# Optimization experiments

Hardware: AMD Instinct MI355X
Metric: run time of the kernel (lower is better)

The kernel has to match this reference:

```python
import jax, jax.numpy as jnp
import numpy as np

B, N, C = 8, 2048, 64  # batch, num nodes, channels
DENSITY = 0.01


def setup_inputs() -> dict:
    key = jax.random.key(0)
    k = jax.random.split(key, 8)
    x = jax.random.normal(k[0], (B, N, C), dtype=jnp.float32)

    # --- replicate sym_norm_Adj(Adj_matrix) + row softmax from __init__ ---
    W = (jax.random.uniform(k[1], (N, N)) < DENSITY).astype(jnp.float32)
    W = W + 0.5 * jnp.eye(N, dtype=jnp.float32)          # W + 0.5*I
    deg = jnp.sum((W != 0.0).astype(jnp.float32), axis=1)  # row nonzero counts
    A = jnp.sqrt(deg)[:, None] * W * jnp.sqrt(deg)[None, :]  # sqrt(D) W sqrt(D)
    A = jax.nn.softmax(A, axis=1)

    s = 1.0 / np.sqrt(C)
    Wq = jax.random.normal(k[2], (C, C), dtype=jnp.float32) * s   # stored as (in,out)
    Wk = jax.random.normal(k[3], (C, C), dtype=jnp.float32) * s
    Wv = jax.random.normal(k[4], (C, N), dtype=jnp.float32) * s   # c_in -> num_node
    theta_w = jax.random.normal(k[5], (C, C), dtype=jnp.float32) * s
    theta_b = jnp.zeros((C,), dtype=jnp.float32)
    alpha = jnp.array([0.95], dtype=jnp.float32)
    beta = jnp.array([0.95], dtype=jnp.float32)
    return {"x": x, "A": A, "Wq": Wq, "Wk": Wk, "Wv": Wv,
            "theta_w": theta_w, "theta_b": theta_b, "alpha": alpha, "beta": beta}


def reference(x, A, Wq, Wk, Wv, theta_w, theta_b, alpha, beta):
    # Spatial_Attention_layer
    Q = x @ Wq                                   # (B,N,C)
    K = x @ Wk                                   # (B,N,C)
    V = x @ Wv                                   # (B,N,N)
    score = jnp.einsum('bnc,bmc->bnm', Q, K)     # (B,N,N)
    score = jax.nn.softmax(score, axis=1)        # softmax over dim=1 (as in torch code)
    spat = jnp.einsum('bnm,bmk->bnk', score, V)  # (B,N,N) spatial attention

    # einsum('nn,bnc->bnc', A, x) == diag(A) broadcast-multiply
    static_out = jnp.diagonal(A)[None, :, None] * x  # (B,N,C)

    # dy_adj = A @ spat; einsum('bnn,bnc->bnc', dy_adj, x) uses only diag(dy_adj)
    dy_diag = jnp.einsum('nj,bjn->bn', A, spat)      # (B,N), avoids (B,N,N) intermediate
    dy_out = (dy_diag[:, :, None] * x) @ theta_w + theta_b  # Theta1 linear

    out = jax.nn.relu(alpha[0] * static_out + beta[0] * dy_out)
    return out
```

## Files before the change

### kernel.cpp

```cpp
#include <hip/hip_runtime.h>

constexpr int Bb = 8;
constexpr int Nn = 2048;
constexpr int Cc = 64;
constexpr int CAPS = 192;

typedef __attribute__((ext_vector_type(4))) float f32x4;
typedef __attribute__((ext_vector_type(16))) float f32x16;
typedef __attribute__((ext_vector_type(8))) short bf16x8;
typedef __attribute__((ext_vector_type(4))) unsigned u32x4;

__device__ inline unsigned short f2bf(float f){
  unsigned u = __builtin_bit_cast(unsigned, f);
  unsigned r = (u + 0x7FFFu + ((u>>16)&1u)) >> 16;
  return (unsigned short)r;
}
__device__ inline float bf2f(unsigned short h){
  unsigned u = ((unsigned)h)<<16; return __builtin_bit_cast(float,u);
}
__device__ inline unsigned pk2(float a, float b){
  return (unsigned)f2bf(a) | ((unsigned)f2bf(b)<<16);
}

typedef __attribute__((address_space(1))) unsigned GU32;
typedef __attribute__((address_space(3))) unsigned LU32;
__device__ inline void load_lds16(const void* g, void* l){
  __builtin_amdgcn_global_load_lds((const GU32*)g, (LU32*)l, 16, 0, 0);
}

__device__ inline size_t qk_chunk(int b, int s, int q, int l){
  return ((((size_t)b*64 + s)*4 + q)*64 + l)*8;
}
__device__ inline size_t xz_chunk(int b, int mq, int cb, int l){
  return ((((size_t)b*128 + mq)*2 + cb)*64 + l)*8;
}

#define MFMA32(a,b,c) __builtin_amdgcn_mfma_f32_32x32x16_bf16(a,b,c,0,0,0)

__global__ __launch_bounds__(256) void mega_k(
    const float* __restrict__ x, const float* __restrict__ A,
    const float* __restrict__ Wq, const float* __restrict__ Wk,
    const float* __restrict__ Tw, const float* __restrict__ Wv,
    unsigned short* __restrict__ Qhi, unsigned short* __restrict__ Qlo,
    unsigned short* __restrict__ Khi, unsigned short* __restrict__ Klo,
    float* __restrict__ xt, float* __restrict__ Xp,
    float* __restrict__ r_, float* __restrict__ diagA, int* __restrict__ cnt,
    int* __restrict__ idx, float* __restrict__ val,
    float* __restrict__ WvT, unsigned short* __restrict__ xf){
  __shared__ __attribute__((aligned(16))) char smem[65792];
  int blk = blockIdx.x; int t = threadIdx.x;

  if(blk < 256){
    float* wql = (float*)smem;
    float* wkl = wql + 4096;
    float* twl = wkl + 4096;
    float (*xr)[64] = (float(*)[64])(twl + 4096);
    float* xsl = (float*)(xr + 64);
    #pragma unroll
    for(int i=0;i<4;i++){
      *(f32x4*)&wql[i*1024+t*4] = *(const f32x4*)&Wq[i*1024+t*4];
      *(f32x4*)&wkl[i*1024+t*4] = *(const f32x4*)&Wk[i*1024+t*4];
      *(f32x4*)&twl[i*1024+t*4] = *(const f32x4*)&Tw[i*1024+t*4];
    }
    if(t<64) xsl[t]=0.f;
    long long row0 = (long long)blk*64;
    int r = t>>4, q = t&15, c0 = q*4;
    #pragma unroll
    for(int i=0;i<4;i++){
      int row = i*16 + r;
      *(f32x4*)&xr[row][c0] = *(const f32x4*)&x[(row0+row)*Cc + c0];
    }
    __syncthreads();
    f32x4 aq[4], ak[4], at4[4];
    #pragma unroll
    for(int g=0;g<4;g++){ aq[g]=(f32x4){0,0,0,0}; ak[g]=(f32x4){0,0,0,0}; at4[g]=(f32x4){0,0,0,0}; }
    for(int kk=0;kk<64;kk++){
      f32x4 wq4 = *(const f32x4*)&wql[kk*64+c0];
      f32x4 wk4 = *(const f32x4*)&wkl[kk*64+c0];
      f32x4 wt4 = *(const f32x4*)&twl[kk*64+c0];
      #pragma unroll
      for(int g=0;g<4;g++){
        float xv = xr[g*16+r][kk];
        aq[g] += xv*wq4; ak[g] += xv*wk4; at4[g] += xv*wt4;
      }
    }
    float xsp[4] = {0.f,0.f,0.f,0.f};
    int q2 = c0>>4, hb = (c0>>3)&1, cs = c0&7;
    #pragma unroll
    for(int g=0;g<4;g++){
      #pragma unroll
      for(int d=0;d<4;d++) xsp[d] += xr[g*16+r][c0+d];
      long long rg = row0 + g*16 + r;
      unsigned long long hq=0,lq=0,hk=0,lk=0;
      #pragma unroll
      for(int d=0;d<4;d++){
        float v = aq[g][d];
        unsigned short h = f2bf(v); unsigned short lo2 = f2bf(v - bf2f(h));
        hq |= (unsigned long long)h << (16*d); lq |= (unsigned long long)lo2 << (16*d);
        v = ak[g][d];
        h = f2bf(v); lo2 = f2bf(v - bf2f(h));
        hk |= (unsigned long long)h << (16*d); lk |= (unsigned long long)lo2 << (16*d);
      }
      int b2 = (int)(rg>>11); int s2 = ((int)rg>>5)&63;
      int l2 = ((int)rg&31) + 32*hb;
      size_t off = qk_chunk(b2, s2, q2, l2) + cs;
      *(unsigned long long*)&Qhi[off] = hq;
      *(unsigned long long*)&Qlo[off] = lq;
      *(unsigned long long*)&Khi[off] = hk;
      *(unsigned long long*)&Klo[off] = lk;
      *(f32x4*)&xt[rg*Cc + c0] = at4[g];
    }
    __syncthreads();
    #pragma unroll
    for(int d=0;d<4;d++) atomicAdd(&xsl[c0+d], xsp[d]);
    __syncthreads();
    if(t<64) Xp[blk*64+t] = xsl[t];
    {
      int b2 = blk>>5; int m0 = (blk&31)*64;
      #pragma unroll
      for(int i=0;i<2;i++){
        int k2 = i*256 + t; int mg2 = k2>>6; int c = k2&63;
        int mloc = mg2*8;
        unsigned u0 = pk2(xr[mloc+0][c], xr[mloc+1][c]);
        unsigned u1 = pk2(xr[mloc+2][c], xr[mloc+3][c]);
        unsigned u2 = pk2(xr[mloc+4][c], xr[mloc+5][c]);
        unsigned u3 = pk2(xr[mloc+6][c], xr[mloc+7][c]);
        u32x4 uu = {u0,u1,u2,u3};
        int mq = (m0 + mloc)>>4; int cb = c>>5; int l2 = (c&31) + 32*(mg2&1);
        *(u32x4*)(xf + xz_chunk(b2, mq, cb, l2)) = uu;
      }
    }
  } else if(blk < 768){
    int n = (blk-256)*4 + (t>>6); int l = t&63;
    const float* row = A + (size_t)n*Nn;
    float mn = 1e30f;
    for(int j=l;j<Nn;j+=64) mn = fminf(mn, row[j]);
    #pragma unroll
    for(int off=32;off>=1;off>>=1) mn = fminf(mn, __shfl_xor(mn,off));
    float thr = mn*1.3f;
    int bse=0;
    for(int j0=0;j0<Nn;j0+=64){
      float v = row[j0+l];
      bool f = v>thr;
      unsigned long long m = __ballot(f);
      int pos = __popcll(m & ((1ull<<l)-1ull));
      if(f && bse+pos<CAPS){ idx[n*CAPS+bse+pos]=j0+l; val[n*CAPS+bse+pos]=v-mn; }
      bse += __popcll(m);
    }
    if(l==0){ r_[n]=mn; diagA[n]=row[n]; cnt[n] = bse<CAPS? bse : CAPS; }
  } else {
    float (*tile)[65] = (float(*)[65])smem;
    int n0 = (blk-768)*64;
    for(int i=0;i<16;i++){
      int cc = i*4 + (t>>6); int nn2 = t&63;
      tile[cc][nn2] = Wv[(size_t)cc*Nn + n0 + nn2];
    }
    __syncthreads();
    for(int i=0;i<16;i++){
      int nn2 = i*4 + (t>>6); int cc = t&63;
      WvT[(size_t)(n0+nn2)*Cc + cc] = tile[cc][nn2];
    }
  }
}

__global__ __launch_bounds__(256,2) void zpass_k(
    const unsigned short* __restrict__ Qhi, const unsigned short* __restrict__ Qlo,
    const unsigned short* __restrict__ Khi, const unsigned short* __restrict__ Klo,
    float* __restrict__ Zp){
  __shared__ uint4 stg[2][512];
  int id = blockIdx.x;
  int b = id&7; int mg = (id>>3)&15; int jq = id>>7;
  int t = threadIdx.x, w = t>>6, l = t&63;
  int mt = mg*4 + w;
  bf16x8 Kh[4], Kl4[4];
  #pragma unroll
  for(int q=0;q<4;q++){
    Kh[q]  = *(const bf16x8*)(Khi + qk_chunk(b, mt, q, l));
    Kl4[q] = *(const bf16x8*)(Klo + qk_chunk(b, mt, q, l));
  }
  char* wbase0 = (char*)&stg[0][0] + (t>>6)*1024;
  char* wbase1 = (char*)&stg[1][0] + (t>>6)*1024;
  {
    int s = jq*8;
    load_lds16(Qhi + qk_chunk(b,s,0,0) + t*8, wbase0);
    load_lds16(Qlo + qk_chunk(b,s,0,0) + t*8, wbase0 + 4096);
  }
  __syncthreads();
  float zacc = 0.f;
  for(int it=0; it<8; it++){
    int buf = it&1;
    if(it+1<8){
      int s = jq*8 + it + 1;
      char* wb = buf? wbase0 : wbase1;
      load_lds16(Qhi + qk_chunk(b,s,0,0) + t*8, wb);
      load_lds16(Qlo + qk_chunk(b,s,0,0) + t*8, wb + 4096);
    }
    f32x16 sa, sb;
    #pragma unroll
    for(int r=0;r<16;r++){ sa[r]=0.f; sb[r]=0.f; }
    #pragma unroll
    for(int q=0;q<4;q++){
      bf16x8 Qh4 = *(const bf16x8*)&stg[buf][q*64 + l];
      bf16x8 Ql4 = *(const bf16x8*)&stg[buf][256 + q*64 + l];
      sa = MFMA32(Qh4, Kh[q],  sa);
      sb = MFMA32(Ql4, Kh[q],  sb);
      sb = MFMA32(Qh4, Kl4[q], sb);
    }
    float p = 0.f;
    #pragma unroll
    for(int r=0;r<16;r++) p += __expf(sa[r]+sb[r]);
    zacc += p;
    __syncthreads();
  }
  zacc += __shfl_down(zacc, 32);
  if(l<32) Zp[((size_t)(jq*8 + b))*Nn + mt*32 + l] = zacc;
}

__global__ __launch_bounds__(256,2) void fused_k(
    const unsigned short* __restrict__ Qhi, const unsigned short* __restrict__ Qlo,
    const unsigned short* __restrict__ Khi, const unsigned short* __restrict__ Klo,
    const unsigned short* __restrict__ xf, const float* __restrict__ Zp,
    float* __restrict__ Pp){
  __shared__ uint4 stg[2][768];
  __shared__ float lniz[256];
  int id = blockIdx.x;
  int b = id&7; int jb = (id>>3)&15; int mo = id>>7;
  int t = threadIdx.x, w = t>>6, l = t&63, lr = l&31, hh = l>>5;
  int js = jb*4 + w;
  {
    int m = mo*256 + t;
    float z = 0.f;
    #pragma unroll
    for(int p=0;p<8;p++) z += Zp[((size_t)(p*8 + b))*Nn + m];
    lniz[t] = -__logf(z);
  }
  bf16x8 Qh4[4], Ql4[4];
  #pragma unroll
  for(int q=0;q<4;q++){
    Qh4[q] = *(const bf16x8*)(Qhi + qk_chunk(b, js, q, l));
    Ql4[q] = *(const bf16x8*)(Qlo + qk_chunk(b, js, q, l));
  }
  char* wbase0 = (char*)&stg[0][0] + (t>>6)*1024;
  char* wbase1 = (char*)&stg[1][0] + (t>>6)*1024;
  {
    int s = mo*8;
    load_lds16(Khi + qk_chunk(b,s,0,0) + t*8, wbase0);
    load_lds16(Klo + qk_chunk(b,s,0,0) + t*8, wbase0 + 4096);
    load_lds16(xf + xz_chunk(b,2*s,0,0) + t*8, wbase0 + 8192);
  }
  __syncthreads();
  f32x16 pa0, pa1;
  #pragma unroll
  for(int r=0;r<16;r++){ pa0[r]=0.f; pa1[r]=0.f; }
  for(int it=0; it<8; it++){
    int buf = it&1;
    if(it+1<8){
      int s = mo*8 + it + 1;
      char* wb = buf? wbase0 : wbase1;
      load_lds16(Khi + qk_chunk(b,s,0,0) + t*8, wb);
      load_lds16(Klo + qk_chunk(b,s,0,0) + t*8, wb + 4096);
      load_lds16(xf + xz_chunk(b,2*s,0,0) + t*8, wb + 8192);
    }
    f32x16 sa, sb;
    #pragma unroll
    for(int r=0;r<16;r++){ sa[r]=0.f; sb[r]=0.f; }
    #pragma unroll
    for(int q=0;q<4;q++){
      bf16x8 Kh4 = *(const bf16x8*)&stg[buf][q*64 + l];
      bf16x8 Kl4 = *(const bf16x8*)&stg[buf][256 + q*64 + l];
      sa = MFMA32(Kh4, Qh4[q], sa);
      sb = MFMA32(Kl4, Qh4[q], sb);
      sb = MFMA32(Kh4, Ql4[q], sb);
    }
    bf16x8 b00 = *(const bf16x8*)&stg[buf][512 + l];
    bf16x8 b10 = *(const bf16x8*)&stg[buf][512 + 64 + l];
    bf16x8 b01 = *(const bf16x8*)&stg[buf][512 + 128 + l];
    bf16x8 b11 = *(const bf16x8*)&stg[buf][512 + 192 + l];
    float e[16];
    #pragma unroll
    for(int r=0;r<16;r++){
      int mrow = (r&3) + 8*(r>>2) + 4*hh;
      e[r] = __expf(sa[r] + sb[r] + lniz[it*32 + mrow]);
    }
    unsigned wd0,wd1,wd2,wd3,wd4,wd5,wd6,wd7;
    {
      unsigned x0 = pk2(e[0],  e[1]);
      unsigned x1 = pk2(e[2],  e[3]);
      unsigned y0 = pk2(e[4],  e[5]);
      unsigned y1 = pk2(e[6],  e[7]);
      asm("v_permlane32_swap_b32 %0, %1" : "+v"(x0), "+v"(y0));
      asm("v_permlane32_swap_b32 %0, %1" : "+v"(x1), "+v"(y1));
      wd0=x0; wd1=x1; wd2=y0; wd3=y1;
      unsigned x2 = pk2(e[8],  e[9]);
      unsigned x3 = pk2(e[10], e[11]);
      unsigned y2 = pk2(e[12], e[13]);
      unsigned y3 = pk2(e[14], e[15]);
      asm("v_permlane32_swap_b32 %0, %1" : "+v"(x2), "+v"(y2));
      asm("v_permlane32_swap_b32 %0, %1" : "+v"(x3), "+v"(y3));
      wd4=x2; wd5=x3; wd6=y2; wd7=y3;
    }
    u32x4 u1 = {wd0,wd1,wd2,wd3};
    u32x4 u2 = {wd4,wd5,wd6,wd7};
    bf16x8 f1 = __builtin_bit_cast(bf16x8, u1);
    bf16x8 f2 = __builtin_bit_cast(bf16x8, u2);
    pa0 = MFMA32(f1, b00, pa0);
    pa0 = MFMA32(f2, b01, pa0);
    pa1 = MFMA32(f1, b10, pa1);
    pa1 = MFMA32(f2, b11, pa1);
    __syncthreads();
  }
  float* Pb = Pp + ((size_t)(mo*8 + b)*Nn + js*32)*Cc;
  #pragma unroll
  for(int r=0;r<16;r++){
    int jr = (r&3) + 8*(r>>2) + 4*hh;
    Pb[(size_t)jr*Cc + lr]      = pa0[r];
    Pb[(size_t)jr*Cc + 32 + lr] = pa1[r];
  }
}

__global__ __launch_bounds__(256) void psum_k(const float* __restrict__ Pp,
                                              float* __restrict__ P){
  size_t i = ((size_t)blockIdx.x*256 + threadIdx.x)*4;
  const size_t st = (size_t)Bb*Nn*Cc;
  f32x4 s0 = *(const f32x4*)(Pp + i)        + *(const f32x4*)(Pp + st + i);
  f32x4 s1 = *(const f32x4*)(Pp + 2*st + i) + *(const f32x4*)(Pp + 3*st + i);
  f32x4 s2 = *(const f32x4*)(Pp + 4*st + i) + *(const f32x4*)(Pp + 5*st + i);
  f32x4 s3 = *(const f32x4*)(Pp + 6*st + i) + *(const f32x4*)(Pp + 7*st + i);
  *(f32x4*)(P + i) = (s0+s1)+(s2+s3);
}

__global__ __launch_bounds__(256) void final_k(const float* __restrict__ x,
    const float* __restrict__ xt, const float* __restrict__ P,
    const float* __restrict__ WvT, const float* __restrict__ Xp,
    const float* __restrict__ r_, const float* __restrict__ diagA,
    const int* __restrict__ cnt, const int* __restrict__ idx,
    const float* __restrict__ val, const float* __restrict__ tb,
    const float* __restrict__ alp, const float* __restrict__ bet,
    float* __restrict__ out){
  int t=threadIdx.x; int l=t&63;
  int bn = blockIdx.x*4 + (t>>6);
  int b = bn>>11, n = bn&2047;
  float wv = WvT[n*Cc+l];
  float xs = 0.f;
  const float* xpb = Xp + (size_t)b*32*Cc;
  #pragma unroll 8
  for(int p=0;p<32;p++) xs += xpb[p*Cc + l];
  float tacc = r_[n]*xs;
  int cn = cnt[n];
  const float* Pb = P + (size_t)b*Nn*Cc;
  const int* ix = idx + n*CAPS;
  const float* vl = val + n*CAPS;
  for(int k=0;k<cn;k++)
    tacc += vl[k] * Pb[(size_t)ix[k]*Cc + l];
  float d = wv*tacc;
  #pragma unroll
  for(int off=32;off>=1;off>>=1) d += __shfl_xor(d,off);
  size_t g = (size_t)bn*Cc + l;
  float o = alp[0]*diagA[n]*x[g] + bet[0]*(d*xt[g] + tb[l]);
  out[g] = fmaxf(o,0.f);
}

extern "C" void kernel_launch(void* const* d_in, const int* in_sizes, int n_in,
                              void* d_out, int out_size, void* d_ws, size_t ws_size,
                              hipStream_t stream){
  const float* x  = (const float*)d_in[0];
  const float* A  = (const float*)d_in[1];
  const float* Wq = (const float*)d_in[2];
  const float* Wk = (const float*)d_in[3];
  const float* Wv = (const float*)d_in[4];
  const float* Tw = (const float*)d_in[5];
  const float* tb = (const float*)d_in[6];
  const float* alp= (const float*)d_in[7];
  const float* bet= (const float*)d_in[8];
  float* out = (float*)d_out;

  char* base = (char*)d_ws; size_t off=0;
  auto al=[&](size_t sz)->void*{ void* q = base+off; off=(off+sz+255)&~(size_t)255; return q; };
  unsigned short* Qhi=(unsigned short*)al((size_t)Bb*Nn*Cc*2);
  unsigned short* Qlo=(unsigned short*)al((size_t)Bb*Nn*Cc*2);
  unsigned short* Khi=(unsigned short*)al((size_t)Bb*Nn*Cc*2);
  unsigned short* Klo=(unsigned short*)al((size_t)Bb*Nn*Cc*2);
  float* xt  =(float*)al((size_t)Bb*Nn*Cc*4);
  float* Pp  =(float*)al((size_t)8*Bb*Nn*Cc*4);
  float* P   =(float*)al((size_t)Bb*Nn*Cc*4);
  float* Zp  =(float*)al((size_t)8*Bb*Nn*4);
  float* Xp  =(float*)al((size_t)256*Cc*4);
  float* WvT =(float*)al((size_t)Nn*Cc*4);
  float* r_  =(float*)al((size_t)Nn*4);
  float* dgA =(float*)al((size_t)Nn*4);
  int*   cnt =(int*)al((size_t)Nn*4);
  int*   idx =(int*)al((size_t)Nn*CAPS*4);
  float* val =(float*)al((size_t)Nn*CAPS*4);
  unsigned short* xf=(unsigned short*)al((size_t)Bb*Cc*Nn*2);
  (void)ws_size;

  mega_k<<<800, 256, 0, stream>>>(x, A, Wq, Wk, Tw, Wv,
      Qhi, Qlo, Khi, Klo, xt, Xp, r_, dgA, cnt, idx, val, WvT, xf);
  zpass_k<<<1024, 256, 0, stream>>>(Qhi,Qlo,Khi,Klo,Zp);
  fused_k<<<1024, 256, 0, stream>>>(Qhi,Qlo,Khi,Klo,xf,Zp,Pp);
  psum_k<<<(int)((size_t)Bb*Nn*Cc/4/256), 256, 0, stream>>>(Pp,P);
  final_k<<<Bb*Nn/4, 256, 0, stream>>>(x,xt,P,WvT,Xp,r_,dgA,cnt,idx,val,tb,alp,bet,out);
}
```

Measured before the change: 109.8 us.

## Triple-buffer LDS prefetch in zpass/fused and halve fused_k m-splits

Both attention passes move from double-buffered LDS staging with a full syncthreads per iteration to a three-stage ring, using explicit vmcnt waits plus a raw s_barrier so two tiles stay in flight. fused_k now processes 16 m-tiles per block instead of 8 and launches half as many blocks. That halves the partial-P buffer and the work left for psum_k, which now sums four slices. The cost is more LDS per block, fewer blocks to fill the GPU, and hand-written waitcnt fences that rely on the exact ordering of async loads.

```diff
diff --git a/kernel.cpp b/kernel.cpp
--- a/kernel.cpp
+++ b/kernel.cpp
@@ -27,6 +27,12 @@
 __device__ inline void load_lds16(const void* g, void* l){
   __builtin_amdgcn_global_load_lds((const GU32*)g, (LU32*)l, 16, 0, 0);
 }
+
+#define PIPE_FENCE_N(N) do{ \
+    asm volatile("s_waitcnt vmcnt(" #N ")" ::: "memory"); \
+    __builtin_amdgcn_sched_barrier(0); \
+    __builtin_amdgcn_s_barrier(); \
+    __builtin_amdgcn_sched_barrier(0); }while(0)
 
 __device__ inline size_t qk_chunk(int b, int s, int q, int l){
   return ((((size_t)b*64 + s)*4 + q)*64 + l)*8;
@@ -167,7 +173,7 @@
     const unsigned short* __restrict__ Qhi, const unsigned short* __restrict__ Qlo,
     const unsigned short* __restrict__ Khi, const unsigned short* __restrict__ Klo,
     float* __restrict__ Zp){
-  __shared__ uint4 stg[2][512];
+  __shared__ uint4 stg[3][512];
   int id = blockIdx.x;
   int b = id&7; int mg = (id>>3)&15; int jq = id>>7;
   int t = threadIdx.x, w = t>>6, l = t&63;
@@ -178,30 +184,24 @@
     Kh[q]  = *(const bf16x8*)(Khi + qk_chunk(b, mt, q, l));
     Kl4[q] = *(const bf16x8*)(Klo + qk_chunk(b, mt, q, l));
   }
-  char* wbase0 = (char*)&stg[0][0] + (t>>6)*1024;
-  char* wbase1 = (char*)&stg[1][0] + (t>>6)*1024;
-  {
-    int s = jq*8;
-    load_lds16(Qhi + qk_chunk(b,s,0,0) + t*8, wbase0);
-    load_lds16(Qlo + qk_chunk(b,s,0,0) + t*8, wbase0 + 4096);
-  }
-  __syncthreads();
+#define ZISSUE(S, BI) { \
+    char* wb = (char*)&stg[BI][0] + ((t>>6)<<10); \
+    load_lds16(Qhi + qk_chunk(b,(S),0,0) + t*8, wb); \
+    load_lds16(Qlo + qk_chunk(b,(S),0,0) + t*8, wb + 4096); }
+  ZISSUE(jq*8,   0);
+  ZISSUE(jq*8+1, 1);
   float zacc = 0.f;
+  #pragma unroll
   for(int it=0; it<8; it++){
-    int buf = it&1;
-    if(it+1<8){
-      int s = jq*8 + it + 1;
-      char* wb = buf? wbase0 : wbase1;
-      load_lds16(Qhi + qk_chunk(b,s,0,0) + t*8, wb);
-      load_lds16(Qlo + qk_chunk(b,s,0,0) + t*8, wb + 4096);
-    }
+    const int bi = it%3;
+    if(it==7) PIPE_FENCE_N(0); else PIPE_FENCE_N(2);
     f32x16 sa, sb;
     #pragma unroll
     for(int r=0;r<16;r++){ sa[r]=0.f; sb[r]=0.f; }
     #pragma unroll
     for(int q=0;q<4;q++){
-      bf16x8 Qh4 = *(const bf16x8*)&stg[buf][q*64 + l];
-      bf16x8 Ql4 = *(const bf16x8*)&stg[buf][256 + q*64 + l];
+      bf16x8 Qh4 = *(const bf16x8*)&stg[bi][q*64 + l];
+      bf16x8 Ql4 = *(const bf16x8*)&stg[bi][256 + q*64 + l];
       sa = MFMA32(Qh4, Kh[q],  sa);
       sb = MFMA32(Ql4, Kh[q],  sb);
       sb = MFMA32(Qh4, Kl4[q], sb);
@@ -210,8 +210,9 @@
     #pragma unroll
     for(int r=0;r<16;r++) p += __expf(sa[r]+sb[r]);
     zacc += p;
-    __syncthreads();
-  }
+    if(it+2<8) ZISSUE(jq*8+it+2, (it+2)%3);
+  }
+#undef ZISSUE
   zacc += __shfl_down(zacc, 32);
   if(l<32) Zp[((size_t)(jq*8 + b))*Nn + mt*32 + l] = zacc;
 }
@@ -221,18 +222,19 @@
     const unsigned short* __restrict__ Khi, const unsigned short* __restrict__ Klo,
     const unsigned short* __restrict__ xf, const float* __restrict__ Zp,
     float* __restrict__ Pp){
-  __shared__ uint4 stg[2][768];
-  __shared__ float lniz[256];
+  __shared__ uint4 stg[3][768];
+  __shared__ float lniz[512];
   int id = blockIdx.x;
   int b = id&7; int jb = (id>>3)&15; int mo = id>>7;
   int t = threadIdx.x, w = t>>6, l = t&63, lr = l&31, hh = l>>5;
   int js = jb*4 + w;
-  {
-    int m = mo*256 + t;
+  #pragma unroll
+  for(int i=0;i<2;i++){
+    int m = mo*512 + i*256 + t;
     float z = 0.f;
     #pragma unroll
     for(int p=0;p<8;p++) z += Zp[((size_t)(p*8 + b))*Nn + m];
-    lniz[t] = -__logf(z);
+    lniz[i*256+t] = -__logf(z);
   }
   bf16x8 Qh4[4], Ql4[4];
   #pragma unroll
@@ -240,42 +242,36 @@
     Qh4[q] = *(const bf16x8*)(Qhi + qk_chunk(b, js, q, l));
     Ql4[q] = *(const bf16x8*)(Qlo + qk_chunk(b, js, q, l));
   }
-  char* wbase0 = (char*)&stg[0][0] + (t>>6)*1024;
-  char* wbase1 = (char*)&stg[1][0] + (t>>6)*1024;
-  {
-    int s = mo*8;
-    load_lds16(Khi + qk_chunk(b,s,0,0) + t*8, wbase0);
-    load_lds16(Klo + qk_chunk(b,s,0,0) + t*8, wbase0 + 4096);
-    load_lds16(xf + xz_chunk(b,2*s,0,0) + t*8, wbase0 + 8192);
-  }
   __syncthreads();
+#define FISSUE(S, BI) { \
+    char* wb = (char*)&stg[BI][0] + ((t>>6)<<10); \
+    load_lds16(Khi + qk_chunk(b,(S),0,0) + t*8, wb); \
+    load_lds16(Klo + qk_chunk(b,(S),0,0) + t*8, wb + 4096); \
+    load_lds16(xf + xz_chunk(b,2*(S),0,0) + t*8, wb + 8192); }
+  FISSUE(mo*16,   0);
+  FISSUE(mo*16+1, 1);
   f32x16 pa0, pa1;
   #pragma unroll
   for(int r=0;r<16;r++){ pa0[r]=0.f; pa1[r]=0.f; }
-  for(int it=0; it<8; it++){
-    int buf = it&1;
-    if(it+1<8){
-      int s = mo*8 + it + 1;
-      char* wb = buf? wbase0 : wbase1;
-      load_lds16(Khi + qk_chunk(b,s,0,0) + t*8, wb);
-      load_lds16(Klo + qk_chunk(b,s,0,0) + t*8, wb + 4096);
-      load_lds16(xf + xz_chunk(b,2*s,0,0) + t*8, wb + 8192);
-    }
+  #pragma unroll
+  for(int it=0; it<16; it++){
+    const int bi = it%3;
+    if(it==15) PIPE_FENCE_N(0); else PIPE_FENCE_N(3);
     f32x16 sa, sb;
     #pragma unroll
     for(int r=0;r<16;r++){ sa[r]=0.f; sb[r]=0.f; }
     #pragma unroll
     for(int q=0;q<4;q++){
-      bf16x8 Kh4 = *(const bf16x8*)&stg[buf][q*64 + l];
-      bf16x8 Kl4 = *(const bf16x8*)&stg[buf][256 + q*64 + l];
+      bf16x8 Kh4 = *(const bf16x8*)&stg[bi][q*64 + l];
+      bf16x8 Kl4 = *(const bf16x8*)&stg[bi][256 + q*64 + l];
       sa = MFMA32(Kh4, Qh4[q], sa);
       sb = MFMA32(Kl4, Qh4[q], sb);
       sb = MFMA32(Kh4, Ql4[q], sb);
     }
-    bf16x8 b00 = *(const bf16x8*)&stg[buf][512 + l];
-    bf16x8 b10 = *(const bf16x8*)&stg[buf][512 + 64 + l];
-    bf16x8 b01 = *(const bf16x8*)&stg[buf][512 + 128 + l];
-    bf16x8 b11 = *(const bf16x8*)&stg[buf][512 + 192 + l];
+    bf16x8 b00 = *(const bf16x8*)&stg[bi][512 + l];
+    bf16x8 b10 = *(const bf16x8*)&stg[bi][512 + 64 + l];
+    bf16x8 b01 = *(const bf16x8*)&stg[bi][512 + 128 + l];
+    bf16x8 b11 = *(const bf16x8*)&stg[bi][512 + 192 + l];
     float e[16];
     #pragma unroll
     for(int r=0;r<16;r++){
@@ -307,8 +303,9 @@
     pa0 = MFMA32(f2, b01, pa0);
     pa1 = MFMA32(f1, b10, pa1);
     pa1 = MFMA32(f2, b11, pa1);
-    __syncthreads();
-  }
+    if(it+2<16) FISSUE(mo*16+it+2, (it+2)%3);
+  }
+#undef FISSUE
   float* Pb = Pp + ((size_t)(mo*8 + b)*Nn + js*32)*Cc;
   #pragma unroll
   for(int r=0;r<16;r++){
@@ -322,11 +319,11 @@
                                               float* __restrict__ P){
   size_t i = ((size_t)blockIdx.x*256 + threadIdx.x)*4;
   const size_t st = (size_t)Bb*Nn*Cc;
-  f32x4 s0 = *(const f32x4*)(Pp + i)        + *(const f32x4*)(Pp + st + i);
-  f32x4 s1 = *(const f32x4*)(Pp + 2*st + i) + *(const f32x4*)(Pp + 3*st + i);
-  f32x4 s2 = *(const f32x4*)(Pp + 4*st + i) + *(const f32x4*)(Pp + 5*st + i);
-  f32x4 s3 = *(const f32x4*)(Pp + 6*st + i) + *(const f32x4*)(Pp + 7*st + i);
-  *(f32x4*)(P + i) = (s0+s1)+(s2+s3);
+  f32x4 a = *(const f32x4*)(Pp + i);
+  f32x4 b = *(const f32x4*)(Pp + st + i);
+  f32x4 c = *(const f32x4*)(Pp + 2*st + i);
+  f32x4 d = *(const f32x4*)(Pp + 3*st + i);
+  *(f32x4*)(P + i) = (a+b)+(c+d);
 }
 
 __global__ __launch_bounds__(256) void final_k(const float* __restrict__ x,
@@ -381,7 +378,7 @@
   unsigned short* Khi=(unsigned short*)al((size_t)Bb*Nn*Cc*2);
   unsigned short* Klo=(unsigned short*)al((size_t)Bb*Nn*Cc*2);
   float* xt  =(float*)al((size_t)Bb*Nn*Cc*4);
-  float* Pp  =(float*)al((size_t)8*Bb*Nn*Cc*4);
+  float* Pp  =(float*)al((size_t)4*Bb*Nn*Cc*4);
   float* P   =(float*)al((size_t)Bb*Nn*Cc*4);
   float* Zp  =(float*)al((size_t)8*Bb*Nn*4);
   float* Xp  =(float*)al((size_t)256*Cc*4);
@@ -392,12 +389,12 @@
   int*   idx =(int*)al((size_t)Nn*CAPS*4);
   float* val =(float*)al((size_t)Nn*CAPS*4);
   unsigned short* xf=(unsigned short*)al((size_t)Bb*Cc*Nn*2);
-  (void)ws_size;
+  (void)ws_size; (void)n_in; (void)in_sizes; (void)out_size;
 
   mega_k<<<800, 256, 0, stream>>>(x, A, Wq, Wk, Tw, Wv,
       Qhi, Qlo, Khi, Klo, xt, Xp, r_, dgA, cnt, idx, val, WvT, xf);
   zpass_k<<<1024, 256, 0, stream>>>(Qhi,Qlo,Khi,Klo,Zp);
-  fused_k<<<1024, 256, 0, stream>>>(Qhi,Qlo,Khi,Klo,xf,Zp,Pp);
+  fused_k<<<512, 256, 0, stream>>>(Qhi,Qlo,Khi,Klo,xf,Zp,Pp);
   psum_k<<<(int)((size_t)Bb*Nn*Cc/4/256), 256, 0, stream>>>(Pp,P);
   final_k<<<Bb*Nn/4, 256, 0, stream>>>(x,xt,P,WvT,Xp,r_,dgA,cnt,idx,val,tb,alp,bet,out);
 }
```

Measured after the change: 107.5 us. 2.0% less time.
